# Optimization experiments

Measured on AMD Instinct MI355X. Metric: run time of the kernel, lower is better.

Reference implementation:

```python
import jax, jax.numpy as jnp
import numpy as np

N = 50000      # graph nodes
E = 400000     # random edges (plus N self-loops)
F = 128        # graph feature dim
H = 4          # GAT heads (layer1)
DH = 64        # gnn_hidden_size (per-head out, layer1)
EMB = 8        # emb_size / GAT final out
B = 16384      # batch
NS = 20        # number of sparse features
V = 1000       # vocab per sparse feature
DENSE = 64     # num_fea_size
HID = 256      # hidden_dims
EPS = 1e-5


def setup_inputs():
    key = jax.random.key(0)
    ks = jax.random.split(key, 40)
    loop = jnp.arange(N, dtype=jnp.int32)
    src = jnp.concatenate([jax.random.randint(ks[0], (E,), 0, N, dtype=jnp.int32), loop])
    dst = jnp.concatenate([jax.random.randint(ks[1], (E,), 0, N, dtype=jnp.int32), loop])
    s = 0.05
    d = {
        'X_id': jax.random.randint(ks[2], (B, 2), 0, N),
        'X_sparse': jax.random.randint(ks[3], (B, NS), 0, V),
        'X_dense': jax.random.normal(ks[4], (B, DENSE), jnp.float32),
        'emb_tables': jax.random.normal(ks[5], (NS, V, EMB), jnp.float32) * s,
        'graph_feature': jax.random.normal(ks[6], (N, F), jnp.float32),
        'src': src, 'dst': dst,
        'wide_w': jax.random.normal(ks[7], (EMB, DENSE), jnp.float32) * s,
        'wide_b': jnp.zeros((EMB,), jnp.float32),
        'lin1_w': jax.random.normal(ks[8], (HID, NS * EMB + DENSE), jnp.float32) * s,
        'lin1_b': jnp.zeros((HID,), jnp.float32),
        'bn1_g': jnp.ones((HID,), jnp.float32),
        'bn1_b': jnp.zeros((HID,), jnp.float32),
        'bn1_m': jax.random.normal(ks[9], (HID,), jnp.float32) * s,
        'bn1_v': jnp.ones((HID,), jnp.float32),
        'lin2_w': jax.random.normal(ks[10], (HID, HID), jnp.float32) * s,
        'lin2_b': jnp.zeros((HID,), jnp.float32),
        'bn2_g': jnp.ones((HID,), jnp.float32),
        'bn2_b': jnp.zeros((HID,), jnp.float32),
        'bn2_m': jax.random.normal(ks[11], (HID,), jnp.float32) * s,
        'bn2_v': jnp.ones((HID,), jnp.float32),
        'dnn_w': jax.random.normal(ks[12], (EMB, HID), jnp.float32) * s,
        'dnn_b': jnp.zeros((EMB,), jnp.float32),
        'gat1_w': jax.random.normal(ks[13], (H * DH, F), jnp.float32) * s,
        'gat1_al': jax.random.normal(ks[14], (H, DH), jnp.float32) * s,
        'gat1_ar': jax.random.normal(ks[15], (H, DH), jnp.float32) * s,
        'gat1_bias': jnp.zeros((H * DH,), jnp.float32),
        'gat2_w': jax.random.normal(ks[16], (EMB, H * DH), jnp.float32) * s,
        'gat2_al': jax.random.normal(ks[17], (1, EMB), jnp.float32) * s,
        'gat2_ar': jax.random.normal(ks[18], (1, EMB), jnp.float32) * s,
        'gat2_bias': jnp.zeros((EMB,), jnp.float32),
        'g1w': jax.random.normal(ks[19], (1, EMB), jnp.float32) * s,
        'g1b': jnp.zeros((1,), jnp.float32),
        'g2w': jax.random.normal(ks[20], (1, EMB), jnp.float32) * s,
        'g2b': jnp.zeros((1,), jnp.float32),
        'g3w': jax.random.normal(ks[21], (1, EMB), jnp.float32) * s,
        'g3b': jnp.zeros((1,), jnp.float32),
        'gout_w': jax.random.normal(ks[22], (2, 3 * EMB), jnp.float32) * s,
        'gout_b': jnp.zeros((2,), jnp.float32),
    }
    return d


def gat_conv(h, W, al, ar, bias, src, dst, heads, dh):
    # DGL GATConv: project, per-edge attention, edge-softmax over dst, aggregate
    feat = (h @ W.T).reshape(-1, heads, dh)          # [N, H, D]
    el = (feat * al).sum(-1)                          # [N, H] src score
    er = (feat * ar).sum(-1)                          # [N, H] dst score
    e = jax.nn.leaky_relu(el[src] + er[dst], 0.2)     # [Etot, H]
    emax = jax.lax.stop_gradient(jax.ops.segment_max(e, dst, num_segments=N))
    a = jnp.exp(e - emax[dst])
    denom = jax.ops.segment_sum(a, dst, num_segments=N)  # [N, H]
    alpha = a / denom[dst]                            # [Etot, H]
    out = jax.ops.segment_sum(alpha[:, :, None] * feat[src], dst, num_segments=N)
    return out + bias.reshape(1, heads, dh)           # [N, H, D]


def batchnorm_eval(x, g, b, m, v):
    return g * (x - m) * jax.lax.rsqrt(v + EPS) + b


def reference(X_id, X_sparse, X_dense, emb_tables, graph_feature, src, dst,
              wide_w, wide_b, lin1_w, lin1_b, bn1_g, bn1_b, bn1_m, bn1_v,
              lin2_w, lin2_b, bn2_g, bn2_b, bn2_m, bn2_v, dnn_w, dnn_b,
              gat1_w, gat1_al, gat1_ar, gat1_bias, gat2_w, gat2_al, gat2_ar, gat2_bias,
              g1w, g1b, g2w, g2b, g3w, g3b, gout_w, gout_b):
    commit_ids = X_id[:, 1]
    # sparse embedding lookup: [B, NS, EMB] -> [B, NS*EMB]
    sparse_embed = emb_tables[jnp.arange(NS)[None, :], X_sparse].reshape(B, NS * EMB)
    x = jnp.concatenate([sparse_embed, X_dense], axis=-1)
    wide_out = X_dense @ wide_w.T + wide_b            # [B, EMB]
    # deep MLP (eval-mode BN, dropout = identity)
    d = jax.nn.relu(batchnorm_eval(x @ lin1_w.T + lin1_b, bn1_g, bn1_b, bn1_m, bn1_v))
    d = jax.nn.relu(batchnorm_eval(d @ lin2_w.T + lin2_b, bn2_g, bn2_b, bn2_m, bn2_v))
    deep_out = d @ dnn_w.T + dnn_b                    # [B, EMB]
    # GAT
    h1 = gat_conv(graph_feature, gat1_w, gat1_al, gat1_ar, gat1_bias, src, dst, H, DH)
    h1 = jax.nn.elu(h1.reshape(N, H * DH))
    h2 = gat_conv(h1, gat2_w, gat2_al, gat2_ar, gat2_bias, src, dst, 1, EMB)
    gcn = h2.reshape(N, EMB)                          # squeeze head dim
    gcn_out = gcn[commit_ids]                         # [B, EMB]
    # Gate (concat)
    aw = jax.nn.sigmoid(wide_out @ g1w.T + g1b)
    bw = jax.nn.sigmoid(deep_out @ g2w.T + g2b)
    cw = jax.nn.sigmoid(gcn_out @ g3w.T + g3b)
    tot = aw + bw + cw
    combined = jnp.concatenate([(aw / tot) * wide_out, (bw / tot) * deep_out,
                                (cw / tot) * gcn_out], axis=1)
    out = combined @ gout_w.T + gout_b                # [B, 2]
    return jax.nn.softmax(out, axis=1)
```

## Files before the change

### kernel.cpp

```cpp
#include <hip/hip_runtime.h>

#define TPB 256
#define DCAP 64
constexpr float BN_EPS = 1e-5f;

typedef __attribute__((ext_vector_type(8))) short short8;
typedef __attribute__((ext_vector_type(4))) float floatx4;

__device__ __forceinline__ float sigmoidf_(float x) { return 1.f / (1.f + __expf(-x)); }
__device__ __forceinline__ unsigned short f2bf(float f) {
    unsigned u = __float_as_uint(f);
    u += 0x7FFFu + ((u >> 16) & 1u);
    return (unsigned short)(u >> 16);
}
__device__ __forceinline__ float bf2f(unsigned short h) {
    return __uint_as_float((unsigned)h << 16);
}


template<bool BNRELU>
__device__ __forceinline__ void gemm_dev(
    const unsigned short* __restrict__ A, const unsigned short* __restrict__ W,
    const float* __restrict__ bias,
    const float* __restrict__ g, const float* __restrict__ bb,
    const float* __restrict__ bm, const float* __restrict__ bv,
    unsigned short* __restrict__ C, int M, int N, int K, int m0, int n0,
    unsigned short* As, unsigned short* Bs)
{
    constexpr int SK = 40;
    int tid = threadIdx.x;
    int wave = tid >> 6, lane = tid & 63;
    int wm = (wave & 1) * 32, wn = (wave >> 1) * 32;
    int lrow = lane & 15, lk = (lane >> 4) * 8;
    floatx4 acc[2][2] = {};
    for (int k0 = 0; k0 < K; k0 += 32) {
        {
            int r = tid >> 2, seg = (tid & 3) * 8;
            uint4 av = make_uint4(0u, 0u, 0u, 0u);
            int gm = m0 + r;
            if (gm < M) av = *(const uint4*)(A + (size_t)gm * K + k0 + seg);
            *(uint4*)(As + r * SK + seg) = av;
            uint4 wv = make_uint4(0u, 0u, 0u, 0u);
            int gn = n0 + r;
            if (gn < N) wv = *(const uint4*)(W + (size_t)gn * K + k0 + seg);
            *(uint4*)(Bs + r * SK + seg) = wv;
        }
        __syncthreads();
        short8 af[2], bfr[2];
#pragma unroll
        for (int i = 0; i < 2; ++i)
            af[i] = *(const short8*)(As + (wm + i * 16 + lrow) * SK + lk);
#pragma unroll
        for (int j = 0; j < 2; ++j)
            bfr[j] = *(const short8*)(Bs + (wn + j * 16 + lrow) * SK + lk);
#pragma unroll
        for (int i = 0; i < 2; ++i)
#pragma unroll
            for (int j = 0; j < 2; ++j)
                acc[i][j] = __builtin_amdgcn_mfma_f32_16x16x32_bf16(
                    af[i], bfr[j], acc[i][j], 0, 0, 0);
        __syncthreads();
    }
    int crow = (lane >> 4) * 4, ccol = lane & 15;
#pragma unroll
    for (int j = 0; j < 2; ++j) {
        int gn = n0 + wn + j * 16 + ccol;
        float sc = 1.f, sh = 0.f;
        if (BNRELU) {
            sc = g[gn] * rsqrtf(bv[gn] + BN_EPS);
            sh = (bias[gn] - bm[gn]) * sc + bb[gn];
        }
#pragma unroll
        for (int i = 0; i < 2; ++i) {
#pragma unroll
            for (int r = 0; r < 4; ++r) {
                int gm = m0 + wm + i * 16 + crow + r;
                if (gm >= M) continue;
                float t = acc[i][j][r];
                if (BNRELU) t = fmaxf(t * sc + sh, 0.f);
                C[(size_t)gm * N + gn] = f2bf(t);
            }
        }
    }
}

__global__ __launch_bounds__(TPB) void stageA_kernel(
    const int* __restrict__ src, const int* __restrict__ dst,
    int* __restrict__ cnt, int* __restrict__ esrc, int E, int sblk,
    const float* __restrict__ w1, unsigned short* __restrict__ o1,
    const float* __restrict__ w2, unsigned short* __restrict__ o2,
    const float* __restrict__ w3, unsigned short* __restrict__ o3,
    const float* __restrict__ gfeat, unsigned short* __restrict__ gfeatb, int ng4,
    const int* __restrict__ Xs, const float* __restrict__ Xd,
    const float* __restrict__ emb, unsigned short* __restrict__ x, int nx)
{
    if ((int)blockIdx.x < sblk) {
        int i = blockIdx.x * TPB + threadIdx.x;
        if (i >= E) return;
        int d = dst[i];
        int pos = atomicAdd(&cnt[d], 1);
        if (pos < DCAP) esrc[(size_t)d * DCAP + pos] = src[i];
        return;
    }
    const int NW = 256 * 224 + 256 * 256 + 256 * 128;
    int idx = (blockIdx.x - sblk) * TPB + threadIdx.x;
    if (idx < NW) {
        if (idx < 256 * 224) o1[idx] = f2bf(w1[idx]);
        else if (idx < 256 * 224 + 256 * 256) o2[idx - 256 * 224] = f2bf(w2[idx - 256 * 224]);
        else o3[idx - 256 * 224 - 256 * 256] = f2bf(w3[idx - 256 * 224 - 256 * 256]);
        return;
    }
    int i = idx - NW;
    if (i < ng4) {
        float4 v = ((const float4*)gfeat)[i];
        ushort4 o;
        o.x = f2bf(v.x); o.y = f2bf(v.y); o.z = f2bf(v.z); o.w = f2bf(v.w);
        ((ushort4*)gfeatb)[i] = o;
        return;
    }
    i -= ng4;
    if (i >= nx) return;
    int b = i / 224, c = i - b * 224;
    float v;
    if (c < 160) {
        int s = c >> 3, j = c & 7;
        int e = Xs[b * 20 + s];
        v = emb[((size_t)s * 1000 + e) * 8 + j];
    } else {
        v = Xd[b * 64 + (c - 160)];
    }
    x[i] = f2bf(v);
}

__global__ __launch_bounds__(256) void stageB_kernel(
    const unsigned short* __restrict__ xb, const unsigned short* __restrict__ w1b,
    const float* __restrict__ lin1_b,
    const float* __restrict__ bn1_g, const float* __restrict__ bn1_b,
    const float* __restrict__ bn1_m, const float* __restrict__ bn1_v,
    unsigned short* __restrict__ d1, int B, int mb1,
    const unsigned short* __restrict__ gfeatb, const unsigned short* __restrict__ wg1b,
    unsigned short* __restrict__ feat1, int Nn, int mbf)
{
    __shared__ unsigned short As[64 * 40];
    __shared__ unsigned short Bs[64 * 40];
    int bid = blockIdx.x;
    int nblk1 = mb1 * 4;
    if (bid < nblk1) {
        int bx = bid % mb1, by = bid / mb1;
        gemm_dev<true>(xb, w1b, lin1_b, bn1_g, bn1_b, bn1_m, bn1_v,
                       d1, B, 256, 224, bx * 64, by * 64, As, Bs);
    } else {
        int b2 = bid - nblk1;
        int bx = b2 % mbf, by = b2 / mbf;
        gemm_dev<false>(gfeatb, wg1b, nullptr, nullptr, nullptr, nullptr, nullptr,
                        feat1, Nn, 256, 128, bx * 64, by * 64, As, Bs);
    }
}

__global__ __launch_bounds__(256) void stageC_kernel(
    const unsigned short* __restrict__ d1, const unsigned short* __restrict__ w2b,
    const float* __restrict__ lin2_b,
    const float* __restrict__ bn2_g, const float* __restrict__ bn2_b,
    const float* __restrict__ bn2_m, const float* __restrict__ bn2_v,
    unsigned short* __restrict__ d2, int B, int mb1,
    const unsigned short* __restrict__ feat1,
    const float* __restrict__ al, const float* __restrict__ ar,
    float* __restrict__ el, float* __restrict__ er, int Nn)
{
    __shared__ unsigned short As[64 * 40];
    __shared__ unsigned short Bs[64 * 40];
    int bid = blockIdx.x;
    int nblk2 = mb1 * 4;
    if (bid < nblk2) {
        int bx = bid % mb1, by = bid / mb1;
        gemm_dev<true>(d1, w2b, lin2_b, bn2_g, bn2_b, bn2_m, bn2_v,
                       d2, B, 256, 256, bx * 64, by * 64, As, Bs);
        return;
    }
    int idx = (bid - nblk2) * TPB + threadIdx.x;
    if (idx >= Nn * 4) return;
    int n = idx >> 2, h = idx & 3;
    const uint2* f4 = (const uint2*)(feat1 + (size_t)n * 256 + h * 64);
    const float4* al4 = (const float4*)(al + h * 64);
    const float4* ar4 = (const float4*)(ar + h * 64);
    float sl = 0.f, sr = 0.f;
#pragma unroll
    for (int d = 0; d < 16; ++d) {
        uint2 fb = f4[d];
        float f0 = bf2f((unsigned short)(fb.x & 0xFFFFu));
        float f1 = bf2f((unsigned short)(fb.x >> 16));
        float f2 = bf2f((unsigned short)(fb.y & 0xFFFFu));
        float f3 = bf2f((unsigned short)(fb.y >> 16));
        float4 lv = al4[d], rv = ar4[d];
        sl += f0 * lv.x + f1 * lv.y + f2 * lv.z + f3 * lv.w;
        sr += f0 * rv.x + f1 * rv.y + f2 * rv.z + f3 * rv.w;
    }
    el[idx] = sl; er[idx] = sr;
}

__global__ __launch_bounds__(TPB) void stageD_kernel(
    const float* __restrict__ Xd, const float* __restrict__ Ww,
    const float* __restrict__ wb, float* __restrict__ wide,
    const unsigned short* __restrict__ d2, const float* __restrict__ Wd,
    const float* __restrict__ db, float* __restrict__ deep, int B, int hblk,
    const unsigned short* __restrict__ feat, const float* __restrict__ el,
    const float* __restrict__ er, const int* __restrict__ cnt,
    const int* __restrict__ esrc, const float* __restrict__ bias,
    const float* __restrict__ w2g, const float* __restrict__ al2,
    const float* __restrict__ ar2,
    float* __restrict__ feat2, float* __restrict__ el2, float* __restrict__ er2, int Nn)
{
    int lane = threadIdx.x & 63;
    if ((int)blockIdx.x < hblk) {
        int nb = (B + 3) / 4;
        float p[8];
        if ((int)blockIdx.x < nb) {
            int r = blockIdx.x * 4 + (threadIdx.x >> 6);
            if (r >= B) return;
            float a = Xd[(size_t)r * 64 + lane];
#pragma unroll
            for (int j = 0; j < 8; ++j) p[j] = a * Ww[j * 64 + lane];
#pragma unroll
            for (int off = 1; off < 64; off <<= 1)
#pragma unroll
                for (int j = 0; j < 8; ++j) p[j] += __shfl_xor(p[j], off, 64);
            if (lane == 0) {
#pragma unroll
                for (int j = 0; j < 8; ++j) wide[(size_t)r * 8 + j] = p[j] + wb[j];
            }
        } else {
            int r = (blockIdx.x - nb) * 4 + (threadIdx.x >> 6);
            if (r >= B) return;
            uint2 ab = *(const uint2*)(d2 + (size_t)r * 256 + lane * 4);
            float a0 = bf2f((unsigned short)(ab.x & 0xFFFFu));
            float a1 = bf2f((unsigned short)(ab.x >> 16));
            float a2 = bf2f((unsigned short)(ab.y & 0xFFFFu));
            float a3 = bf2f((unsigned short)(ab.y >> 16));
#pragma unroll
            for (int j = 0; j < 8; ++j) {
                float4 wv = *(const float4*)(Wd + j * 256 + lane * 4);
                p[j] = a0 * wv.x + a1 * wv.y + a2 * wv.z + a3 * wv.w;
            }
#pragma unroll
            for (int off = 1; off < 64; off <<= 1)
#pragma unroll
                for (int j = 0; j < 8; ++j) p[j] += __shfl_xor(p[j], off, 64);
            if (lane == 0) {
#pragma unroll
                for (int j = 0; j < 8; ++j) deep[(size_t)r * 8 + j] = p[j] + db[j];
            }
        }
        return;
    }
    int n = (blockIdx.x - hblk) * 4 + (threadIdx.x >> 6);
    if (n >= Nn) return;
    int h = lane >> 4;
    int c = h * 64 + (lane & 15) * 4;
    float erv = er[n * 4 + h];
    int beg = n * DCAP;
    int deg = cnt[n]; if (deg > DCAP) deg = DCAP;
    int end = beg + deg;
    float4 acc = make_float4(0.f, 0.f, 0.f, 0.f);
    float dsum = 0.f;
    int e = beg;
    for (; e + 4 <= end; e += 4) {
        int sv[4]; float lv[4]; uint2 fb[4];
#pragma unroll
        for (int u = 0; u < 4; ++u) sv[u] = esrc[e + u];
#pragma unroll
        for (int u = 0; u < 4; ++u) lv[u] = el[sv[u] * 4 + h];
#pragma unroll
        for (int u = 0; u < 4; ++u) fb[u] = *(const uint2*)(feat + (size_t)sv[u] * 256 + c);
#pragma unroll
        for (int u = 0; u < 4; ++u) {
            float ev = lv[u] + erv;
            ev = ev > 0.f ? ev : 0.2f * ev;
            float av = __expf(ev);
            dsum += av;
            acc.x += av * bf2f((unsigned short)(fb[u].x & 0xFFFFu));
            acc.y += av * bf2f((unsigned short)(fb[u].x >> 16));
            acc.z += av * bf2f((unsigned short)(fb[u].y & 0xFFFFu));
            acc.w += av * bf2f((unsigned short)(fb[u].y >> 16));
        }
    }
    for (; e < end; ++e) {
        int s = esrc[e];
        float ev = el[s * 4 + h] + erv;
        ev = ev > 0.f ? ev : 0.2f * ev;
        float av = __expf(ev);
        dsum += av;
        uint2 fb = *(const uint2*)(feat + (size_t)s * 256 + c);
        acc.x += av * bf2f((unsigned short)(fb.x & 0xFFFFu));
        acc.y += av * bf2f((unsigned short)(fb.x >> 16));
        acc.z += av * bf2f((unsigned short)(fb.y & 0xFFFFu));
        acc.w += av * bf2f((unsigned short)(fb.y >> 16));
    }
    float inv = 1.f / dsum;
    float4 bv = *(const float4*)(bias + c);
    float4 o;
    o.x = acc.x * inv + bv.x; o.y = acc.y * inv + bv.y;
    o.z = acc.z * inv + bv.z; o.w = acc.w * inv + bv.w;
    o.x = o.x > 0.f ? o.x : __expf(o.x) - 1.f;
    o.y = o.y > 0.f ? o.y : __expf(o.y) - 1.f;
    o.z = o.z > 0.f ? o.z : __expf(o.z) - 1.f;
    o.w = o.w > 0.f ? o.w : __expf(o.w) - 1.f;
    float p[8];
#pragma unroll
    for (int j = 0; j < 8; ++j) {
        float4 wv = *(const float4*)(w2g + j * 256 + c);
        p[j] = o.x * wv.x + o.y * wv.y + o.z * wv.z + o.w * wv.w;
    }
#pragma unroll
    for (int off = 1; off < 64; off <<= 1)
#pragma unroll
        for (int j = 0; j < 8; ++j)
            p[j] += __shfl_xor(p[j], off, 64);
    if (lane == 0) {
        float e_l = 0.f, e_r = 0.f;
#pragma unroll
        for (int j = 0; j < 8; ++j) {
            feat2[(size_t)n * 8 + j] = p[j];
            e_l += p[j] * al2[j];
            e_r += p[j] * ar2[j];
        }
        el2[n] = e_l; er2[n] = e_r;
    }
}

__global__ __launch_bounds__(TPB) void gat2_final_kernel(
    const float* __restrict__ feat2, const float* __restrict__ el,
    const float* __restrict__ er, const int* __restrict__ cnt,
    const int* __restrict__ esrc, const int* __restrict__ Xid,
    const float* __restrict__ wide, const float* __restrict__ deep,
    const float* __restrict__ g2bias,
    const float* __restrict__ g1w, const float* __restrict__ g1b,
    const float* __restrict__ g2w, const float* __restrict__ g2b,
    const float* __restrict__ g3w, const float* __restrict__ g3b,
    const float* __restrict__ goutw, const float* __restrict__ goutb,
    float* __restrict__ out, int B)
{
    __shared__ float ls[256];
    int tid = threadIdx.x;
    int b = blockIdx.x * 32 + (tid >> 3), j = tid & 7;
    if (b < B) {
        int n = Xid[b * 2 + 1];
        float erv = er[n];
        int beg = n * DCAP;
        int deg = cnt[n]; if (deg > DCAP) deg = DCAP;
        int end = beg + deg;
        float acc = 0.f, dsum = 0.f;
        int e = beg;
        for (; e + 4 <= end; e += 4) {
            int sv[4]; float lv[4], fv[4];
#pragma unroll
            for (int u = 0; u < 4; ++u) sv[u] = esrc[e + u];
#pragma unroll
            for (int u = 0; u < 4; ++u) lv[u] = el[sv[u]];
#pragma unroll
            for (int u = 0; u < 4; ++u) fv[u] = feat2[(size_t)sv[u] * 8 + j];
#pragma unroll
            for (int u = 0; u < 4; ++u) {
                float ev = lv[u] + erv;
                ev = ev > 0.f ? ev : 0.2f * ev;
                float av = __expf(ev);
                dsum += av;
                acc += av * fv[u];
            }
        }
        for (; e < end; ++e) {
            int s = esrc[e];
            float ev = el[s] + erv;
            ev = ev > 0.f ? ev : 0.2f * ev;
            float av = __expf(ev);
            dsum += av;
            acc += av * feat2[(size_t)s * 8 + j];
        }
        ls[tid] = acc / dsum + g2bias[j];
    }
    __syncthreads();
    if (tid >= 32) return;
    int br = blockIdx.x * 32 + tid;
    if (br >= B) return;
    float w8[8], d8[8], g8[8];
    {
        float4 t0 = *(const float4*)(wide + (size_t)br * 8);
        float4 t1 = *(const float4*)(wide + (size_t)br * 8 + 4);
        w8[0] = t0.x; w8[1] = t0.y; w8[2] = t0.z; w8[3] = t0.w;
        w8[4] = t1.x; w8[5] = t1.y; w8[6] = t1.z; w8[7] = t1.w;
        t0 = *(const float4*)(deep + (size_t)br * 8);
        t1 = *(const float4*)(deep + (size_t)br * 8 + 4);
        d8[0] = t0.x; d8[1] = t0.y; d8[2] = t0.z; d8[3] = t0.w;
        d8[4] = t1.x; d8[5] = t1.y; d8[6] = t1.z; d8[7] = t1.w;
#pragma unroll
        for (int j2 = 0; j2 < 8; ++j2) g8[j2] = ls[tid * 8 + j2];
    }
    float s1 = g1b[0], s2 = g2b[0], s3 = g3b[0];
#pragma unroll
    for (int j2 = 0; j2 < 8; ++j2) { s1 += w8[j2] * g1w[j2]; s2 += d8[j2] * g2w[j2]; s3 += g8[j2] * g3w[j2]; }
    float aw = sigmoidf_(s1), bw = sigmoidf_(s2), cw = sigmoidf_(s3);
    float inv_tot = 1.f / (aw + bw + cw);
    float an = aw * inv_tot, bn = bw * inv_tot, cn = cw * inv_tot;
    float o0 = goutb[0], o1 = goutb[1];
#pragma unroll
    for (int j2 = 0; j2 < 8; ++j2) {
        float c0 = an * w8[j2]; o0 += goutw[j2] * c0;      o1 += goutw[24 + j2] * c0;
        float c1 = bn * d8[j2]; o0 += goutw[8 + j2] * c1;  o1 += goutw[32 + j2] * c1;
        float c2 = cn * g8[j2]; o0 += goutw[16 + j2] * c2; o1 += goutw[40 + j2] * c2;
    }
    float mx = fmaxf(o0, o1);
    float e0 = __expf(o0 - mx), e1 = __expf(o1 - mx);
    float inv = 1.f / (e0 + e1);
    out[(size_t)br * 2] = e0 * inv;
    out[(size_t)br * 2 + 1] = e1 * inv;
}

extern "C" void kernel_launch(void* const* d_in, const int* in_sizes, int n_in,
                              void* d_out, int out_size, void* d_ws, size_t ws_size,
                              hipStream_t stream)
{
    const int*   Xid    = (const int*)d_in[0];
    const int*   Xs     = (const int*)d_in[1];
    const float* Xd     = (const float*)d_in[2];
    const float* emb    = (const float*)d_in[3];
    const float* gfeat  = (const float*)d_in[4];
    const int*   src    = (const int*)d_in[5];
    const int*   dst    = (const int*)d_in[6];
    const float* wide_w = (const float*)d_in[7];
    const float* wide_b = (const float*)d_in[8];
    const float* lin1_w = (const float*)d_in[9];
    const float* lin1_b = (const float*)d_in[10];
    const float* bn1_g  = (const float*)d_in[11];
    const float* bn1_b  = (const float*)d_in[12];
    const float* bn1_m  = (const float*)d_in[13];
    const float* bn1_v  = (const float*)d_in[14];
    const float* lin2_w = (const float*)d_in[15];
    const float* lin2_b = (const float*)d_in[16];
    const float* bn2_g  = (const float*)d_in[17];
    const float* bn2_b  = (const float*)d_in[18];
    const float* bn2_m  = (const float*)d_in[19];
    const float* bn2_v  = (const float*)d_in[20];
    const float* dnn_w  = (const float*)d_in[21];
    const float* dnn_b  = (const float*)d_in[22];
    const float* gat1_w = (const float*)d_in[23];
    const float* gat1_al = (const float*)d_in[24];
    const float* gat1_ar = (const float*)d_in[25];
    const float* gat1_bias = (const float*)d_in[26];
    const float* gat2_w = (const float*)d_in[27];
    const float* gat2_al = (const float*)d_in[28];
    const float* gat2_ar = (const float*)d_in[29];
    const float* gat2_bias = (const float*)d_in[30];
    const float* g1w = (const float*)d_in[31];
    const float* g1b = (const float*)d_in[32];
    const float* g2w = (const float*)d_in[33];
    const float* g2b = (const float*)d_in[34];
    const float* g3w = (const float*)d_in[35];
    const float* g3b = (const float*)d_in[36];
    const float* goutw = (const float*)d_in[37];
    const float* goutb = (const float*)d_in[38];

    const int B    = in_sizes[0] / 2;
    const int Nn   = in_sizes[4] / 128;
    const int Etot = in_sizes[5];

    char* base = (char*)d_ws;
    size_t off = 0;
    auto alloc = [&](size_t bytes) -> char* {
        char* p = base + off;
        off += (bytes + 255) & ~(size_t)255;
        return p;
    };
    unsigned short* xb = (unsigned short*)alloc((size_t)B * 224 * 2);
    unsigned short* d1 = (unsigned short*)alloc((size_t)B * 256 * 2);
    unsigned short* d2 = (unsigned short*)alloc((size_t)B * 256 * 2);
    unsigned short* feat1  = (unsigned short*)alloc((size_t)Nn * 256 * 2);
    unsigned short* gfeatb = (unsigned short*)alloc((size_t)Nn * 128 * 2);
    unsigned short* w1b = (unsigned short*)alloc(256 * 224 * 2);
    unsigned short* w2b = (unsigned short*)alloc(256 * 256 * 2);
    unsigned short* wg1b = (unsigned short*)alloc(256 * 128 * 2);
    float* wide  = (float*)alloc((size_t)B * 8 * 4);
    float* deep  = (float*)alloc((size_t)B * 8 * 4);
    float* el1   = (float*)alloc((size_t)Nn * 4 * 4);
    float* er1   = (float*)alloc((size_t)Nn * 4 * 4);
    float* feat2 = (float*)alloc((size_t)Nn * 8 * 4);
    float* el2   = (float*)alloc((size_t)Nn * 4);
    float* er2   = (float*)alloc((size_t)Nn * 4);
    int* cnt     = (int*)alloc((size_t)Nn * 4);
    int* esrc    = (int*)alloc((size_t)Nn * DCAP * 4);

    hipMemsetAsync(cnt, 0, (size_t)Nn * sizeof(int), stream);

    {
        const int sblk = (Etot + TPB - 1) / TPB;
        const int NW = 256 * 224 + 256 * 256 + 256 * 128;
        const int NG4 = Nn * 128 / 4;
        const int NX = B * 224;
        const int pblk = (NW + NG4 + NX + TPB - 1) / TPB;
        stageA_kernel<<<sblk + pblk, TPB, 0, stream>>>(
            src, dst, cnt, esrc, Etot, sblk,
            lin1_w, w1b, lin2_w, w2b, gat1_w, wg1b,
            gfeat, gfeatb, NG4, Xs, Xd, emb, xb, NX);
    }

    const int mb1 = (B + 63) / 64;
    const int mbf = (Nn + 63) / 64;

    stageB_kernel<<<mb1 * 4 + mbf * 4, 256, 0, stream>>>(
        xb, w1b, lin1_b, bn1_g, bn1_b, bn1_m, bn1_v, d1, B, mb1,
        gfeatb, wg1b, feat1, Nn, mbf);

    {
        const int ablk = (Nn * 4 + TPB - 1) / TPB;
        stageC_kernel<<<mb1 * 4 + ablk, 256, 0, stream>>>(
            d1, w2b, lin2_b, bn2_g, bn2_b, bn2_m, bn2_v, d2, B, mb1,
            feat1, gat1_al, gat1_ar, el1, er1, Nn);
    }

    {
        const int hblk = 2 * ((B + 3) / 4);
        const int gblk = (Nn + 3) / 4;
        stageD_kernel<<<hblk + gblk, TPB, 0, stream>>>(
            Xd, wide_w, wide_b, wide, d2, dnn_w, dnn_b, deep, B, hblk,
            feat1, el1, er1, cnt, esrc, gat1_bias,
            gat2_w, gat2_al, gat2_ar, feat2, el2, er2, Nn);
    }

    gat2_final_kernel<<<(B + 31) / 32, TPB, 0, stream>>>(
        feat2, el2, er2, cnt, esrc, Xid, wide, deep, gat2_bias,
        g1w, g1b, g2w, g2b, g3w, g3b, goutw, goutb, (float*)d_out, B);
}
```

Baseline: 291.4 us.

## Replace shared-memory block GEMM with per-wave direct-from-global MFMA tiles

The 64x64 block-tiled GEMM that staged A and W tiles through LDS with two barriers per k-step is replaced by independent per-wave 32x32 tiles that load MFMA fragments directly from global memory. The aim is to remove LDS traffic and synchronisation overhead and to raise the number of independent work units. In exchange, data reuse across waves is lost, so each operand is re-fetched from global or L2 more often and the loads are narrower per lane. Out-of-range rows are handled by clamping the row index.

```diff
diff --git a/kernel.cpp b/kernel.cpp
--- a/kernel.cpp
+++ b/kernel.cpp
@@ -17,54 +17,42 @@
     return __uint_as_float((unsigned)h << 16);
 }
 
-
 template<bool BNRELU>
-__device__ __forceinline__ void gemm_dev(
+__device__ __forceinline__ void gemm_wave(
     const unsigned short* __restrict__ A, const unsigned short* __restrict__ W,
     const float* __restrict__ bias,
     const float* __restrict__ g, const float* __restrict__ bb,
     const float* __restrict__ bm, const float* __restrict__ bv,
-    unsigned short* __restrict__ C, int M, int N, int K, int m0, int n0,
-    unsigned short* As, unsigned short* Bs)
-{
-    constexpr int SK = 40;
-    int tid = threadIdx.x;
-    int wave = tid >> 6, lane = tid & 63;
-    int wm = (wave & 1) * 32, wn = (wave >> 1) * 32;
+    unsigned short* __restrict__ C, int M, int N, int K, int m0, int n0)
+{
+    int lane = threadIdx.x & 63;
     int lrow = lane & 15, lk = (lane >> 4) * 8;
     floatx4 acc[2][2] = {};
+#pragma unroll 2
     for (int k0 = 0; k0 < K; k0 += 32) {
-        {
-            int r = tid >> 2, seg = (tid & 3) * 8;
-            uint4 av = make_uint4(0u, 0u, 0u, 0u);
-            int gm = m0 + r;
-            if (gm < M) av = *(const uint4*)(A + (size_t)gm * K + k0 + seg);
-            *(uint4*)(As + r * SK + seg) = av;
-            uint4 wv = make_uint4(0u, 0u, 0u, 0u);
-            int gn = n0 + r;
-            if (gn < N) wv = *(const uint4*)(W + (size_t)gn * K + k0 + seg);
-            *(uint4*)(Bs + r * SK + seg) = wv;
-        }
-        __syncthreads();
         short8 af[2], bfr[2];
 #pragma unroll
-        for (int i = 0; i < 2; ++i)
-            af[i] = *(const short8*)(As + (wm + i * 16 + lrow) * SK + lk);
-#pragma unroll
-        for (int j = 0; j < 2; ++j)
-            bfr[j] = *(const short8*)(Bs + (wn + j * 16 + lrow) * SK + lk);
+        for (int i = 0; i < 2; ++i) {
+            int gm = m0 + i * 16 + lrow;
+            gm = gm < M ? gm : M - 1;
+            af[i] = *(const short8*)(A + (size_t)gm * K + k0 + lk);
+        }
+#pragma unroll
+        for (int j = 0; j < 2; ++j) {
+            int gn = n0 + j * 16 + lrow;
+            bfr[j] = *(const short8*)(W + (size_t)gn * K + k0 + lk);
+        }
 #pragma unroll
         for (int i = 0; i < 2; ++i)
 #pragma unroll
             for (int j = 0; j < 2; ++j)
                 acc[i][j] = __builtin_amdgcn_mfma_f32_16x16x32_bf16(
                     af[i], bfr[j], acc[i][j], 0, 0, 0);
-        __syncthreads();
     }
     int crow = (lane >> 4) * 4, ccol = lane & 15;
 #pragma unroll
     for (int j = 0; j < 2; ++j) {
-        int gn = n0 + wn + j * 16 + ccol;
+        int gn = n0 + j * 16 + ccol;
         float sc = 1.f, sh = 0.f;
         if (BNRELU) {
             sc = g[gn] * rsqrtf(bv[gn] + BN_EPS);
@@ -74,7 +62,7 @@
         for (int i = 0; i < 2; ++i) {
 #pragma unroll
             for (int r = 0; r < 4; ++r) {
-                int gm = m0 + wm + i * 16 + crow + r;
+                int gm = m0 + i * 16 + crow + r;
                 if (gm >= M) continue;
                 float t = acc[i][j][r];
                 if (BNRELU) t = fmaxf(t * sc + sh, 0.f);
@@ -137,23 +125,21 @@
     const float* __restrict__ lin1_b,
     const float* __restrict__ bn1_g, const float* __restrict__ bn1_b,
     const float* __restrict__ bn1_m, const float* __restrict__ bn1_v,
-    unsigned short* __restrict__ d1, int B, int mb1,
+    unsigned short* __restrict__ d1, int B, int mt1,
     const unsigned short* __restrict__ gfeatb, const unsigned short* __restrict__ wg1b,
-    unsigned short* __restrict__ feat1, int Nn, int mbf)
-{
-    __shared__ unsigned short As[64 * 40];
-    __shared__ unsigned short Bs[64 * 40];
-    int bid = blockIdx.x;
-    int nblk1 = mb1 * 4;
-    if (bid < nblk1) {
-        int bx = bid % mb1, by = bid / mb1;
-        gemm_dev<true>(xb, w1b, lin1_b, bn1_g, bn1_b, bn1_m, bn1_v,
-                       d1, B, 256, 224, bx * 64, by * 64, As, Bs);
+    unsigned short* __restrict__ feat1, int Nn, int mtf)
+{
+    int w = blockIdx.x * 4 + (threadIdx.x >> 6);
+    int nw1 = mt1 * 8;
+    if (w < nw1) {
+        int mt = w % mt1, nt = w / mt1;
+        gemm_wave<true>(xb, w1b, lin1_b, bn1_g, bn1_b, bn1_m, bn1_v,
+                        d1, B, 256, 224, mt * 32, nt * 32);
     } else {
-        int b2 = bid - nblk1;
-        int bx = b2 % mbf, by = b2 / mbf;
-        gemm_dev<false>(gfeatb, wg1b, nullptr, nullptr, nullptr, nullptr, nullptr,
-                        feat1, Nn, 256, 128, bx * 64, by * 64, As, Bs);
+        int w2 = w - nw1;
+        int mt = w2 % mtf, nt = w2 / mtf;
+        gemm_wave<false>(gfeatb, wg1b, nullptr, nullptr, nullptr, nullptr, nullptr,
+                         feat1, Nn, 256, 128, mt * 32, nt * 32);
     }
 }
 
@@ -162,22 +148,19 @@
     const float* __restrict__ lin2_b,
     const float* __restrict__ bn2_g, const float* __restrict__ bn2_b,
     const float* __restrict__ bn2_m, const float* __restrict__ bn2_v,
-    unsigned short* __restrict__ d2, int B, int mb1,
+    unsigned short* __restrict__ d2, int B, int mt1, int gblk2,
     const unsigned short* __restrict__ feat1,
     const float* __restrict__ al, const float* __restrict__ ar,
     float* __restrict__ el, float* __restrict__ er, int Nn)
 {
-    __shared__ unsigned short As[64 * 40];
-    __shared__ unsigned short Bs[64 * 40];
-    int bid = blockIdx.x;
-    int nblk2 = mb1 * 4;
-    if (bid < nblk2) {
-        int bx = bid % mb1, by = bid / mb1;
-        gemm_dev<true>(d1, w2b, lin2_b, bn2_g, bn2_b, bn2_m, bn2_v,
-                       d2, B, 256, 256, bx * 64, by * 64, As, Bs);
+    if ((int)blockIdx.x < gblk2) {
+        int w = blockIdx.x * 4 + (threadIdx.x >> 6);
+        int mt = w % mt1, nt = w / mt1;
+        gemm_wave<true>(d1, w2b, lin2_b, bn2_g, bn2_b, bn2_m, bn2_v,
+                        d2, B, 256, 256, mt * 32, nt * 32);
         return;
     }
-    int idx = (bid - nblk2) * TPB + threadIdx.x;
+    int idx = (blockIdx.x - gblk2) * TPB + threadIdx.x;
     if (idx >= Nn * 4) return;
     int n = idx >> 2, h = idx & 3;
     const uint2* f4 = (const uint2*)(feat1 + (size_t)n * 256 + h * 64);
@@ -501,17 +484,21 @@
             gfeat, gfeatb, NG4, Xs, Xd, emb, xb, NX);
     }
 
-    const int mb1 = (B + 63) / 64;
-    const int mbf = (Nn + 63) / 64;
-
-    stageB_kernel<<<mb1 * 4 + mbf * 4, 256, 0, stream>>>(
-        xb, w1b, lin1_b, bn1_g, bn1_b, bn1_m, bn1_v, d1, B, mb1,
-        gfeatb, wg1b, feat1, Nn, mbf);
+    const int mt1 = (B + 31) / 32;
+    const int mtf = (Nn + 31) / 32;
 
     {
+        const int nwaves = mt1 * 8 + mtf * 8;
+        stageB_kernel<<<nwaves / 4, 256, 0, stream>>>(
+            xb, w1b, lin1_b, bn1_g, bn1_b, bn1_m, bn1_v, d1, B, mt1,
+            gfeatb, wg1b, feat1, Nn, mtf);
+    }
+
+    {
+        const int gblk2 = mt1 * 8 / 4;
         const int ablk = (Nn * 4 + TPB - 1) / TPB;
-        stageC_kernel<<<mb1 * 4 + ablk, 256, 0, stream>>>(
-            d1, w2b, lin2_b, bn2_g, bn2_b, bn2_m, bn2_v, d2, B, mb1,
+        stageC_kernel<<<gblk2 + ablk, 256, 0, stream>>>(
+            d1, w2b, lin2_b, bn2_g, bn2_b, bn2_m, bn2_v, d2, B, mt1, gblk2,
             feat1, gat1_al, gat1_ar, el1, er1, Nn);
     }
 
```

Measured after the change: 319.2 us. +9.5%, slower.

## Load GEMM tiles via global_load_lds and move wide linear into stage A

Applied to the files above, without the earlier changes.

The GEMM tile staging now uses direct global-to-LDS DMA loads of 16 bytes per lane instead of loading into registers and then storing to shared memory. The padded LDS row stride is dropped so that each wave's contiguous DMA footprint matches the tile layout. Out-of-range A rows are clamped rather than zero-filled, and the N bound check is removed. The wide linear head moves from stageD into extra blocks of stageA, which shortens stageD. The trade-off is possible LDS bank conflicts from the unpadded layout, and a reliance on correct vmcnt waiting before the barrier.

```diff
diff --git a/kernel.cpp b/kernel.cpp
--- a/kernel.cpp
+++ b/kernel.cpp
@@ -17,6 +17,11 @@
     return __uint_as_float((unsigned)h << 16);
 }
 
+__device__ __forceinline__ void async_load16(const unsigned short* g, unsigned short* l) {
+    __builtin_amdgcn_global_load_lds(
+        (const __attribute__((address_space(1))) void*)g,
+        (__attribute__((address_space(3))) void*)l, 16, 0, 0);
+}
 
 template<bool BNRELU>
 __device__ __forceinline__ void gemm_dev(
@@ -27,24 +32,21 @@
     unsigned short* __restrict__ C, int M, int N, int K, int m0, int n0,
     unsigned short* As, unsigned short* Bs)
 {
-    constexpr int SK = 40;
+    constexpr int SK = 32;
     int tid = threadIdx.x;
     int wave = tid >> 6, lane = tid & 63;
     int wm = (wave & 1) * 32, wn = (wave >> 1) * 32;
     int lrow = lane & 15, lk = (lane >> 4) * 8;
+    int sr = tid >> 2, sc = (tid & 3) * 8;
+    int gmA = m0 + sr; if (gmA >= M) gmA = M - 1;
+    const unsigned short* gA = A + (size_t)gmA * K + sc;
+    const unsigned short* gB = W + (size_t)(n0 + sr) * K + sc;
+    unsigned short* lA = As + wave * 512;
+    unsigned short* lB = Bs + wave * 512;
     floatx4 acc[2][2] = {};
     for (int k0 = 0; k0 < K; k0 += 32) {
-        {
-            int r = tid >> 2, seg = (tid & 3) * 8;
-            uint4 av = make_uint4(0u, 0u, 0u, 0u);
-            int gm = m0 + r;
-            if (gm < M) av = *(const uint4*)(A + (size_t)gm * K + k0 + seg);
-            *(uint4*)(As + r * SK + seg) = av;
-            uint4 wv = make_uint4(0u, 0u, 0u, 0u);
-            int gn = n0 + r;
-            if (gn < N) wv = *(const uint4*)(W + (size_t)gn * K + k0 + seg);
-            *(uint4*)(Bs + r * SK + seg) = wv;
-        }
+        async_load16(gA + k0, lA);
+        async_load16(gB + k0, lB);
         __syncthreads();
         short8 af[2], bfr[2];
 #pragma unroll
@@ -65,10 +67,10 @@
 #pragma unroll
     for (int j = 0; j < 2; ++j) {
         int gn = n0 + wn + j * 16 + ccol;
-        float sc = 1.f, sh = 0.f;
+        float sc2 = 1.f, sh = 0.f;
         if (BNRELU) {
-            sc = g[gn] * rsqrtf(bv[gn] + BN_EPS);
-            sh = (bias[gn] - bm[gn]) * sc + bb[gn];
+            sc2 = g[gn] * rsqrtf(bv[gn] + BN_EPS);
+            sh = (bias[gn] - bm[gn]) * sc2 + bb[gn];
         }
 #pragma unroll
         for (int i = 0; i < 2; ++i) {
@@ -77,7 +79,7 @@
                 int gm = m0 + wm + i * 16 + crow + r;
                 if (gm >= M) continue;
                 float t = acc[i][j][r];
-                if (BNRELU) t = fmaxf(t * sc + sh, 0.f);
+                if (BNRELU) t = fmaxf(t * sc2 + sh, 0.f);
                 C[(size_t)gm * N + gn] = f2bf(t);
             }
         }
@@ -92,7 +94,9 @@
     const float* __restrict__ w3, unsigned short* __restrict__ o3,
     const float* __restrict__ gfeat, unsigned short* __restrict__ gfeatb, int ng4,
     const int* __restrict__ Xs, const float* __restrict__ Xd,
-    const float* __restrict__ emb, unsigned short* __restrict__ x, int nx)
+    const float* __restrict__ emb, unsigned short* __restrict__ x, int nx, int pblk,
+    const float* __restrict__ Ww, const float* __restrict__ wb,
+    float* __restrict__ wide, int B)
 {
     if ((int)blockIdx.x < sblk) {
         int i = blockIdx.x * TPB + threadIdx.x;
@@ -102,34 +106,52 @@
         if (pos < DCAP) esrc[(size_t)d * DCAP + pos] = src[i];
         return;
     }
-    const int NW = 256 * 224 + 256 * 256 + 256 * 128;
-    int idx = (blockIdx.x - sblk) * TPB + threadIdx.x;
-    if (idx < NW) {
-        if (idx < 256 * 224) o1[idx] = f2bf(w1[idx]);
-        else if (idx < 256 * 224 + 256 * 256) o2[idx - 256 * 224] = f2bf(w2[idx - 256 * 224]);
-        else o3[idx - 256 * 224 - 256 * 256] = f2bf(w3[idx - 256 * 224 - 256 * 256]);
+    if ((int)blockIdx.x < sblk + pblk) {
+        const int NW = 256 * 224 + 256 * 256 + 256 * 128;
+        int idx = (blockIdx.x - sblk) * TPB + threadIdx.x;
+        if (idx < NW) {
+            if (idx < 256 * 224) o1[idx] = f2bf(w1[idx]);
+            else if (idx < 256 * 224 + 256 * 256) o2[idx - 256 * 224] = f2bf(w2[idx - 256 * 224]);
+            else o3[idx - 256 * 224 - 256 * 256] = f2bf(w3[idx - 256 * 224 - 256 * 256]);
+            return;
+        }
+        int i = idx - NW;
+        if (i < ng4) {
+            float4 v = ((const float4*)gfeat)[i];
+            ushort4 o;
+            o.x = f2bf(v.x); o.y = f2bf(v.y); o.z = f2bf(v.z); o.w = f2bf(v.w);
+            ((ushort4*)gfeatb)[i] = o;
+            return;
+        }
+        i -= ng4;
+        if (i >= nx) return;
+        int b = i / 224, c = i - b * 224;
+        float v;
+        if (c < 160) {
+            int s = c >> 3, j = c & 7;
+            int e = Xs[b * 20 + s];
+            v = emb[((size_t)s * 1000 + e) * 8 + j];
+        } else {
+            v = Xd[b * 64 + (c - 160)];
+        }
+        x[i] = f2bf(v);
         return;
     }
-    int i = idx - NW;
-    if (i < ng4) {
-        float4 v = ((const float4*)gfeat)[i];
-        ushort4 o;
-        o.x = f2bf(v.x); o.y = f2bf(v.y); o.z = f2bf(v.z); o.w = f2bf(v.w);
-        ((ushort4*)gfeatb)[i] = o;
-        return;
-    }
-    i -= ng4;
-    if (i >= nx) return;
-    int b = i / 224, c = i - b * 224;
-    float v;
-    if (c < 160) {
-        int s = c >> 3, j = c & 7;
-        int e = Xs[b * 20 + s];
-        v = emb[((size_t)s * 1000 + e) * 8 + j];
-    } else {
-        v = Xd[b * 64 + (c - 160)];
-    }
-    x[i] = f2bf(v);
+    int lane = threadIdx.x & 63;
+    int r = (blockIdx.x - sblk - pblk) * 4 + (threadIdx.x >> 6);
+    if (r >= B) return;
+    float a = Xd[(size_t)r * 64 + lane];
+    float p[8];
+#pragma unroll
+    for (int j = 0; j < 8; ++j) p[j] = a * Ww[j * 64 + lane];
+#pragma unroll
+    for (int off = 1; off < 64; off <<= 1)
+#pragma unroll
+        for (int j = 0; j < 8; ++j) p[j] += __shfl_xor(p[j], off, 64);
+    if (lane == 0) {
+#pragma unroll
+        for (int j = 0; j < 8; ++j) wide[(size_t)r * 8 + j] = p[j] + wb[j];
+    }
 }
 
 __global__ __launch_bounds__(256) void stageB_kernel(
@@ -141,8 +163,8 @@
     const unsigned short* __restrict__ gfeatb, const unsigned short* __restrict__ wg1b,
     unsigned short* __restrict__ feat1, int Nn, int mbf)
 {
-    __shared__ unsigned short As[64 * 40];
-    __shared__ unsigned short Bs[64 * 40];
+    __shared__ unsigned short As[64 * 32];
+    __shared__ unsigned short Bs[64 * 32];
     int bid = blockIdx.x;
     int nblk1 = mb1 * 4;
     if (bid < nblk1) {
@@ -167,8 +189,8 @@
     const float* __restrict__ al, const float* __restrict__ ar,
     float* __restrict__ el, float* __restrict__ er, int Nn)
 {
-    __shared__ unsigned short As[64 * 40];
-    __shared__ unsigned short Bs[64 * 40];
+    __shared__ unsigned short As[64 * 32];
+    __shared__ unsigned short Bs[64 * 32];
     int bid = blockIdx.x;
     int nblk2 = mb1 * 4;
     if (bid < nblk2) {
@@ -199,8 +221,6 @@
 }
 
 __global__ __launch_bounds__(TPB) void stageD_kernel(
-    const float* __restrict__ Xd, const float* __restrict__ Ww,
-    const float* __restrict__ wb, float* __restrict__ wide,
     const unsigned short* __restrict__ d2, const float* __restrict__ Wd,
     const float* __restrict__ db, float* __restrict__ deep, int B, int hblk,
     const unsigned short* __restrict__ feat, const float* __restrict__ el,
@@ -212,43 +232,26 @@
 {
     int lane = threadIdx.x & 63;
     if ((int)blockIdx.x < hblk) {
-        int nb = (B + 3) / 4;
+        int r = blockIdx.x * 4 + (threadIdx.x >> 6);
+        if (r >= B) return;
         float p[8];
-        if ((int)blockIdx.x < nb) {
-            int r = blockIdx.x * 4 + (threadIdx.x >> 6);
-            if (r >= B) return;
-            float a = Xd[(size_t)r * 64 + lane];
-#pragma unroll
-            for (int j = 0; j < 8; ++j) p[j] = a * Ww[j * 64 + lane];
-#pragma unroll
-            for (int off = 1; off < 64; off <<= 1)
-#pragma unroll
-                for (int j = 0; j < 8; ++j) p[j] += __shfl_xor(p[j], off, 64);
-            if (lane == 0) {
-#pragma unroll
-                for (int j = 0; j < 8; ++j) wide[(size_t)r * 8 + j] = p[j] + wb[j];
-            }
-        } else {
-            int r = (blockIdx.x - nb) * 4 + (threadIdx.x >> 6);
-            if (r >= B) return;
-            uint2 ab = *(const uint2*)(d2 + (size_t)r * 256 + lane * 4);
-            float a0 = bf2f((unsigned short)(ab.x & 0xFFFFu));
-            float a1 = bf2f((unsigned short)(ab.x >> 16));
-            float a2 = bf2f((unsigned short)(ab.y & 0xFFFFu));
-            float a3 = bf2f((unsigned short)(ab.y >> 16));
-#pragma unroll
-            for (int j = 0; j < 8; ++j) {
-                float4 wv = *(const float4*)(Wd + j * 256 + lane * 4);
-                p[j] = a0 * wv.x + a1 * wv.y + a2 * wv.z + a3 * wv.w;
-            }
-#pragma unroll
-            for (int off = 1; off < 64; off <<= 1)
-#pragma unroll
-                for (int j = 0; j < 8; ++j) p[j] += __shfl_xor(p[j], off, 64);
-            if (lane == 0) {
-#pragma unroll
-                for (int j = 0; j < 8; ++j) deep[(size_t)r * 8 + j] = p[j] + db[j];
-            }
+        uint2 ab = *(const uint2*)(d2 + (size_t)r * 256 + lane * 4);
+        float a0 = bf2f((unsigned short)(ab.x & 0xFFFFu));
+        float a1 = bf2f((unsigned short)(ab.x >> 16));
+        float a2 = bf2f((unsigned short)(ab.y & 0xFFFFu));
+        float a3 = bf2f((unsigned short)(ab.y >> 16));
+#pragma unroll
+        for (int j = 0; j < 8; ++j) {
+            float4 wv = *(const float4*)(Wd + j * 256 + lane * 4);
+            p[j] = a0 * wv.x + a1 * wv.y + a2 * wv.z + a3 * wv.w;
+        }
+#pragma unroll
+        for (int off = 1; off < 64; off <<= 1)
+#pragma unroll
+            for (int j = 0; j < 8; ++j) p[j] += __shfl_xor(p[j], off, 64);
+        if (lane == 0) {
+#pragma unroll
+            for (int j = 0; j < 8; ++j) deep[(size_t)r * 8 + j] = p[j] + db[j];
         }
         return;
     }
@@ -495,10 +498,12 @@
         const int NG4 = Nn * 128 / 4;
         const int NX = B * 224;
         const int pblk = (NW + NG4 + NX + TPB - 1) / TPB;
-        stageA_kernel<<<sblk + pblk, TPB, 0, stream>>>(
+        const int wblk = (B + 3) / 4;
+        stageA_kernel<<<sblk + pblk + wblk, TPB, 0, stream>>>(
             src, dst, cnt, esrc, Etot, sblk,
             lin1_w, w1b, lin2_w, w2b, gat1_w, wg1b,
-            gfeat, gfeatb, NG4, Xs, Xd, emb, xb, NX);
+            gfeat, gfeatb, NG4, Xs, Xd, emb, xb, NX, pblk,
+            wide_w, wide_b, wide, B);
     }
 
     const int mb1 = (B + 63) / 64;
@@ -516,10 +521,10 @@
     }
 
     {
-        const int hblk = 2 * ((B + 3) / 4);
+        const int hblk = (B + 3) / 4;
         const int gblk = (Nn + 3) / 4;
         stageD_kernel<<<hblk + gblk, TPB, 0, stream>>>(
-            Xd, wide_w, wide_b, wide, d2, dnn_w, dnn_b, deep, B, hblk,
+            d2, dnn_w, dnn_b, deep, B, hblk,
             feat1, el1, er1, cnt, esrc, gat1_bias,
             gat2_w, gat2_al, gat2_ar, feat2, el2, er2, Nn);
     }
```

New measurement: 287.2 us. No clear change (-1.4%).
